# Performance work log

Hardware: AMD Instinct MI355X
Metric: run time of the kernel (lower is better)

The kernel has to match this reference:

```python
import jax, jax.numpy as jnp
import numpy as np

NUM_HEADS = 16
NUM_KV_HEADS = 8
HEAD_DIM = 128
SLIDING_WINDOW = 1024
ROPE_THETA = 10000.0
EPS = 1e-6


def _rms_norm(x, w, eps=EPS):
    # x: [..., head_dim]; Gemma RMSNorm: x * rsqrt(mean(x^2)+eps) * (1 + w)
    var = jnp.mean(jnp.square(x), axis=-1, keepdims=True)
    return x * jax.lax.rsqrt(var + eps) * (1.0 + w)


def _rotate_half(x):
    h = x.shape[-1] // 2
    return jnp.concatenate([-x[..., h:], x[..., :h]], axis=-1)


def _rope_cos_sin(seq_len, dim, theta, dtype):
    inv_freq = 1.0 / (theta ** (jnp.arange(0, dim, 2, dtype=jnp.float32) / dim))
    t = jnp.arange(seq_len, dtype=jnp.float32)
    freqs = jnp.outer(t, inv_freq)              # [S, dim/2]
    emb = jnp.concatenate([freqs, freqs], -1)   # [S, dim]
    return jnp.cos(emb).astype(dtype), jnp.sin(emb).astype(dtype)


def setup_inputs() -> dict:
    key = jax.random.key(0)
    ks = jax.random.split(key, 7)
    B, S, H = 2, 2048, 2048
    std = 0.02
    return {
        "hidden_states": jax.random.normal(ks[0], (B, S, H), jnp.float32),
        "wq": jax.random.normal(ks[1], (NUM_HEADS * HEAD_DIM, H), jnp.float32) * std,
        "wk": jax.random.normal(ks[2], (NUM_KV_HEADS * HEAD_DIM, H), jnp.float32) * std,
        "wv": jax.random.normal(ks[3], (NUM_KV_HEADS * HEAD_DIM, H), jnp.float32) * std,
        "wo": jax.random.normal(ks[4], (H, NUM_HEADS * HEAD_DIM), jnp.float32) * std,
        "q_norm_weight": jnp.zeros((HEAD_DIM,), jnp.float32),
        "k_norm_weight": jnp.zeros((HEAD_DIM,), jnp.float32),
    }


def reference(hidden_states, wq, wk, wv, wo, q_norm_weight, k_norm_weight):
    B, S, H = hidden_states.shape
    # QKV projections (Linear, no bias): x @ W^T
    q = (hidden_states @ wq.T).reshape(B, S, NUM_HEADS, HEAD_DIM).transpose(0, 2, 1, 3)
    k = (hidden_states @ wk.T).reshape(B, S, NUM_KV_HEADS, HEAD_DIM).transpose(0, 2, 1, 3)
    v = (hidden_states @ wv.T).reshape(B, S, NUM_KV_HEADS, HEAD_DIM).transpose(0, 2, 1, 3)
    # QK RMSNorm (per head_dim)
    q = _rms_norm(q, q_norm_weight)
    k = _rms_norm(k, k_norm_weight)
    # RoPE (local layer -> theta=10000)
    cos, sin = _rope_cos_sin(S, HEAD_DIM, ROPE_THETA, q.dtype)  # [S, D]
    q = q * cos + _rotate_half(q) * sin
    k = k * cos + _rotate_half(k) * sin
    # GQA: repeat kv heads (repeat_interleave on head dim)
    groups = NUM_HEADS // NUM_KV_HEADS
    k = jnp.repeat(k, groups, axis=1)
    v = jnp.repeat(v, groups, axis=1)
    # scores [B, H, S, S]
    scale = 1.0 / jnp.sqrt(jnp.asarray(HEAD_DIM, jnp.float32))
    scores = jnp.einsum("bhqd,bhkd->bhqk", q, k) * scale
    # sliding-window causal mask: allowed iff i - window + 1 <= j <= i
    i = jnp.arange(S)[:, None]
    j = jnp.arange(S)[None, :]
    allowed = (j <= i) & (j > i - SLIDING_WINDOW)
    scores = jnp.where(allowed, scores, jnp.float32(-jnp.inf))
    probs = jax.nn.softmax(scores.astype(jnp.float32), axis=-1).astype(q.dtype)
    attn = jnp.einsum("bhqk,bhkd->bhqd", probs, v)  # [B, H, S, D]
    attn = attn.transpose(0, 2, 1, 3).reshape(B, S, NUM_HEADS * HEAD_DIM)
    return attn @ wo.T
```

## Files before the change

### kernel.cpp

```cpp
#include <hip/hip_runtime.h>
#include <stdint.h>
#include <math.h>

typedef unsigned short u16;
typedef __attribute__((ext_vector_type(8))) __bf16 v8bf;
typedef v8bf __attribute__((may_alias)) v8bf_a;
typedef __attribute__((ext_vector_type(4))) float v4f;
typedef __attribute__((ext_vector_type(4))) u16 v4u16;
typedef v4u16 __attribute__((may_alias)) v4u16_a;
typedef __attribute__((ext_vector_type(8))) u16 v8u16;
typedef v8u16 __attribute__((may_alias)) v8u16_a;

__device__ __forceinline__ float bf2f(u16 u) {
    union { uint32_t i; float f; } c; c.i = ((uint32_t)u) << 16; return c.f;
}
__device__ __forceinline__ u16 f2bf(float f) {
    union { float f; uint32_t i; } c; c.f = f;
    return (u16)((c.i + 0x7FFFu + ((c.i >> 16) & 1u)) >> 16);
}
__device__ __forceinline__ void gl_lds16(const u16* g, u16* l) {
    __builtin_amdgcn_global_load_lds(
        (const __attribute__((address_space(1))) void*)g,
        (__attribute__((address_space(3))) void*)l, 16, 0, 0);
}

__global__ __launch_bounds__(256) void convert_bf16(
    const float* __restrict__ src, u16* __restrict__ dst, int n)
{
    const int stride = gridDim.x * blockDim.x;
    for (int i = blockIdx.x * blockDim.x + threadIdx.x; i * 8 < n; i += stride) {
        const int base = i * 8;
        v8u16 o;
#pragma unroll
        for (int j = 0; j < 8; j++) o[j] = f2bf(src[base + j]);
        *(v8u16_a*)(dst + base) = o;
    }
}

template <bool F32OUT>
__global__ __launch_bounds__(256) void gemm_bt(
    const u16* __restrict__ A, int lda,
    const u16* __restrict__ W0, const u16* __restrict__ W1, const u16* __restrict__ W2,
    int n1, int n2, void* __restrict__ Cv, int ldc, int K)
{
    __shared__ __align__(16) u16 As[128 * 32];
    __shared__ __align__(16) u16 Bs[128 * 32];
    const int t  = threadIdx.x;
    const int m0 = blockIdx.x * 128, n0 = blockIdx.y * 128;

    const u16* W; int nw;
    if (n0 < n1)      { W = W0; nw = n0; }
    else if (n0 < n2) { W = W1; nw = n0 - n1; }
    else              { W = W2; nw = n0 - n2; }

    const int lrow = t >> 2, lcol = (t & 3) * 8;
    const u16* gA = A + (size_t)(m0 + lrow) * lda + lcol;
    const u16* gB = W + (size_t)(nw + lrow) * K + lcol;

    const int wid = t >> 6, lane = t & 63;
    const int wm = (wid >> 1) * 64, wn = (wid & 1) * 64;
    const int l15 = lane & 15, quad = lane >> 4;

    v4f acc[4][4] = {};

    for (int k0 = 0; k0 < K; k0 += 32) {
        gl_lds16(gA + k0,                      As + t * 8);
        gl_lds16(gA + k0 + (size_t)64 * lda,   As + 2048 + t * 8);
        gl_lds16(gB + k0,                      Bs + t * 8);
        gl_lds16(gB + k0 + (size_t)64 * K,     Bs + 2048 + t * 8);
        __syncthreads();
        v8bf af[4], bfr[4];
#pragma unroll
        for (int i = 0; i < 4; i++) af[i]  = *(const v8bf_a*)(As + (wm + i * 16 + l15) * 32 + quad * 8);
#pragma unroll
        for (int j = 0; j < 4; j++) bfr[j] = *(const v8bf_a*)(Bs + (wn + j * 16 + l15) * 32 + quad * 8);
#pragma unroll
        for (int i = 0; i < 4; i++)
#pragma unroll
            for (int j = 0; j < 4; j++)
                acc[i][j] = __builtin_amdgcn_mfma_f32_16x16x32_bf16(af[i], bfr[j], acc[i][j], 0, 0, 0);
        __syncthreads();
    }

#pragma unroll
    for (int i = 0; i < 4; i++)
#pragma unroll
        for (int j = 0; j < 4; j++)
#pragma unroll
            for (int r = 0; r < 4; r++) {
                const int row = m0 + wm + i * 16 + quad * 4 + r;
                const int col = n0 + wn + j * 16 + l15;
                if (F32OUT) ((float*)Cv)[(size_t)row * ldc + col] = acc[i][j][r];
                else        ((u16*)Cv)[(size_t)row * ldc + col]   = f2bf(acc[i][j][r]);
            }
}

__global__ __launch_bounds__(256) void normrope(
    u16* __restrict__ qkv, const u16* __restrict__ qw, const u16* __restrict__ kw)
{
    const int tok = blockIdx.x;
    const int s = tok & 2047;
    const int wid = threadIdx.x >> 6, lane = threadIdx.x & 63;
    const int d  = lane * 2;
    const int dm = d & 63;
    const float kln = 9.210340371976184f / 64.f;
    const float inv0 = expf(-(float)dm * kln);
    const float inv1 = expf(-(float)(dm + 1) * kln);
    float sn0, cs0, sn1, cs1;
    __sincosf((float)s * inv0, &sn0, &cs0);
    __sincosf((float)s * inv1, &sn1, &cs1);

    for (int task = wid; task < 24; task += 4) {
        const bool isq = task < 16;
        const int  hh  = isq ? task : task - 16;
        u16* p = qkv + (size_t)tok * 4096 + (isq ? hh * 128 : 2048 + hh * 128) + d;
        const float x0 = bf2f(p[0]), x1 = bf2f(p[1]);
        float ss = x0 * x0 + x1 * x1;
#pragma unroll
        for (int off = 32; off; off >>= 1) ss += __shfl_xor(ss, off);
        const float rr = rsqrtf(ss * (1.f / 128.f) + 1e-6f);
        const u16* wp = (isq ? qw : kw) + d;
        const float xn0 = x0 * rr * (1.f + bf2f(wp[0]));
        const float xn1 = x1 * rr * (1.f + bf2f(wp[1]));
        const float pp0 = __shfl_xor(xn0, 32);
        const float pp1 = __shfl_xor(xn1, 32);
        float o0, o1;
        if (lane < 32) { o0 = xn0 * cs0 - pp0 * sn0; o1 = xn1 * cs1 - pp1 * sn1; }
        else           { o0 = xn0 * cs0 + pp0 * sn0; o1 = xn1 * cs1 + pp1 * sn1; }
        p[0] = f2bf(o0); p[1] = f2bf(o1);
    }
}

__global__ __launch_bounds__(256) void vtrans(
    const u16* __restrict__ qkv, u16* __restrict__ v_t)
{
    __shared__ __align__(16) u16 tile[64][80];
    const int b = blockIdx.x, st = blockIdx.y * 64, ct = blockIdx.z * 64;
    const int t = threadIdx.x;
    {
        const int sl = t >> 2, cq = (t & 3) * 16;
        const u16* src = qkv + ((size_t)(b * 2048 + st + sl)) * 4096 + 3072 + ct + cq;
        *(v8u16_a*)&tile[sl][cq]     = *(const v8u16_a*)src;
        *(v8u16_a*)&tile[sl][cq + 8] = *(const v8u16_a*)(src + 8);
    }
    __syncthreads();
    {
        const int dl = t >> 2, sq = (t & 3) * 16;
        v8u16 o0, o1;
#pragma unroll
        for (int i = 0; i < 8; i++) { o0[i] = tile[sq + i][dl]; o1[i] = tile[sq + 8 + i][dl]; }
        u16* dst = v_t + ((size_t)(b * 1024 + ct + dl)) * 2048 + st + sq;
        *(v8u16_a*)dst       = o0;
        *(v8u16_a*)(dst + 8) = o1;
    }
}

__global__ __launch_bounds__(256) void attn_fa(
    const u16* __restrict__ qkv,
    const u16* __restrict__ v_t,
    u16* __restrict__ attn)
{
    __shared__ __align__(16) u16 Ks[2][32 * 128];
    __shared__ __align__(16) u16 p_lds[4][16 * 72];
    const int bh = blockIdx.x;
    const int b = bh >> 4, h = bh & 15, kvh = h >> 1;
    const int t = threadIdx.x;
    const int wid = t >> 6, lane = t & 63;
    const int l15 = lane & 15, quad = lane >> 4;
    const int qb0 = ((int)gridDim.y - 1 - (int)blockIdx.y) * 64;
    const int qw0 = qb0 + wid * 16;
    const int q   = qw0 + l15;

    const u16* Qb = qkv + ((size_t)(b * 2048 + q)) * 4096 + h * 128 + quad * 8;
    v8bf qf[4];
#pragma unroll
    for (int kc = 0; kc < 4; kc++) qf[kc] = *(const v8bf_a*)(Qb + kc * 32);

    const u16* Kb = qkv + (size_t)b * 2048 * 4096 + 2048 + kvh * 128;
    const u16* Vb = v_t + (size_t)(b * 1024 + kvh * 128) * 2048;

    int ks = qb0 - 1023; if (ks < 0) ks = 0;
    const int kstart = ks & ~31, kend = qb0 + 63;

    const int sr0 = t >> 4, sc = t & 15, sr1 = sr0 + 16;
    const int so0 = (sc ^ (sr0 & 7)) * 8;
    const int so1 = (sc ^ (sr1 & 7)) * 8;

    gl_lds16(Kb + (size_t)(kstart + sr0) * 4096 + so0, &Ks[0][(size_t)t * 8]);
    gl_lds16(Kb + (size_t)(kstart + sr1) * 4096 + so1, &Ks[0][(size_t)(256 + t) * 8]);

    v4f o[8] = {};
    float m_run = -INFINITY;
    float msafe = 0.f;
    float l_i = 0.f;
    const float kSc = 0.08838834764831845f;
    const float THR = 90.50966799187808f;
    u16* P = &p_lds[wid][0];
    const int swz = l15 & 7;

    int buf = 0;
    for (int kt = kstart; kt <= kend; kt += 32, buf ^= 1) {
        __syncthreads();
        if (kt + 32 <= kend) {
            gl_lds16(Kb + (size_t)(kt + 32 + sr0) * 4096 + so0, &Ks[buf ^ 1][(size_t)t * 8]);
            gl_lds16(Kb + (size_t)(kt + 32 + sr1) * 4096 + so1, &Ks[buf ^ 1][(size_t)(256 + t) * 8]);
        }
        if (kt > qw0 + 15 || kt + 31 <= qw0 - 1024) continue;

        v8bf vf[8];
        const u16* Vr = Vb + (size_t)l15 * 2048 + kt + quad * 8;
#pragma unroll
        for (int nt = 0; nt < 8; nt++) vf[nt] = *(const v8bf_a*)(Vr + (size_t)nt * 16 * 2048);

        v4f s0 = {}, s1 = {};
        const u16* K0 = &Ks[buf][(size_t)l15 * 128];
        const u16* K1 = K0 + 16 * 128;
#pragma unroll
        for (int kc = 0; kc < 4; kc++) {
            const int cs = ((kc * 4 + quad) ^ swz) * 8;
            s0 = __builtin_amdgcn_mfma_f32_16x16x32_bf16(*(const v8bf_a*)(K0 + cs), qf[kc], s0, 0, 0, 0);
            s1 = __builtin_amdgcn_mfma_f32_16x16x32_bf16(*(const v8bf_a*)(K1 + cs), qf[kc], s1, 0, 0, 0);
        }

        float p[8];
        float mx = -INFINITY;
#pragma unroll
        for (int r = 0; r < 4; r++) {
            const int kk0 = kt + quad * 4 + r, kk1 = kk0 + 16;
            const float v0 = (kk0 <= q && kk0 > q - 1024) ? s0[r] : -INFINITY;
            const float v1 = (kk1 <= q && kk1 > q - 1024) ? s1[r] : -INFINITY;
            p[r] = v0; p[r + 4] = v1;
            mx = fmaxf(mx, fmaxf(v0, v1));
        }
        mx = fmaxf(mx, __shfl_xor(mx, 16));
        mx = fmaxf(mx, __shfl_xor(mx, 32));

        if (!__all(mx <= m_run + THR)) {
            const float mnew  = fmaxf(m_run, mx);
            const float msn   = (mnew == -INFINITY) ? 0.f : mnew;
            const float alpha = __expf((m_run - msn) * kSc);
#pragma unroll
            for (int nt = 0; nt < 8; nt++)
#pragma unroll
                for (int r = 0; r < 4; r++) o[nt][r] *= alpha;
            l_i *= alpha;
            m_run = mnew; msafe = msn;
        }

        const float mb = msafe * kSc;
        float ps = 0.f;
#pragma unroll
        for (int j = 0; j < 8; j++) {
            p[j] = __expf(__builtin_fmaf(p[j], kSc, -mb));
            ps += p[j];
        }

        union { v4u16 v; uint32_t d[2]; } u0, u1;
        asm("v_cvt_pk_bf16_f32 %0, %1, %2" : "=v"(u0.d[0]) : "v"(p[0]), "v"(p[1]));
        asm("v_cvt_pk_bf16_f32 %0, %1, %2" : "=v"(u0.d[1]) : "v"(p[2]), "v"(p[3]));
        asm("v_cvt_pk_bf16_f32 %0, %1, %2" : "=v"(u1.d[0]) : "v"(p[4]), "v"(p[5]));
        asm("v_cvt_pk_bf16_f32 %0, %1, %2" : "=v"(u1.d[1]) : "v"(p[6]), "v"(p[7]));
        *(v4u16_a*)(P + l15 * 72 + quad * 4)      = u0.v;
        *(v4u16_a*)(P + l15 * 72 + 16 + quad * 4) = u1.v;

        ps += __shfl_xor(ps, 16);
        ps += __shfl_xor(ps, 32);
        l_i += ps;

        asm volatile("s_waitcnt lgkmcnt(0)" ::: "memory");
        const v8bf pf = *(const v8bf_a*)(P + l15 * 72 + quad * 8);
#pragma unroll
        for (int nt = 0; nt < 8; nt++)
            o[nt] = __builtin_amdgcn_mfma_f32_16x16x32_bf16(vf[nt], pf, o[nt], 0, 0, 0);
    }

    const float inv = 1.0f / l_i;
    u16* orow = attn + ((size_t)(b * 2048 + q)) * 2048 + h * 128 + quad * 4;
#pragma unroll
    for (int nt = 0; nt < 8; nt++) {
        v4u16 ov;
#pragma unroll
        for (int r = 0; r < 4; r++) ov[r] = f2bf(o[nt][r] * inv);
        *(v4u16_a*)(orow + nt * 16) = ov;
    }
}

extern "C" void kernel_launch(void* const* d_in, const int* in_sizes, int n_in,
                              void* d_out, int out_size, void* d_ws, size_t ws_size,
                              hipStream_t stream)
{
    u16* qkv  = (u16*)d_ws;
    u16* v_t  = qkv  + (size_t)16777216;
    u16* xa   = v_t  + (size_t)4194304;
    u16* wbf  = xa   + (size_t)8388608;
    u16* nwq  = wbf  + (size_t)8388608;
    u16* nwk  = nwq  + 128;

    convert_bf16<<<4096, 256, 0, stream>>>((const float*)d_in[0], xa,            8388608);
    convert_bf16<<<2048, 256, 0, stream>>>((const float*)d_in[1], wbf,           4194304);
    convert_bf16<<<1024, 256, 0, stream>>>((const float*)d_in[2], wbf + 4194304, 2097152);
    convert_bf16<<<1024, 256, 0, stream>>>((const float*)d_in[3], wbf + 6291456, 2097152);
    convert_bf16<<<1,    256, 0, stream>>>((const float*)d_in[5], nwq,           128);
    convert_bf16<<<1,    256, 0, stream>>>((const float*)d_in[6], nwk,           128);
    gemm_bt<false><<<dim3(32, 32), 256, 0, stream>>>(xa, 2048, wbf, wbf + 4194304, wbf + 6291456,
                                                     2048, 3072, qkv, 4096, 2048);
    convert_bf16<<<2048, 256, 0, stream>>>((const float*)d_in[4], wbf, 4194304);
    normrope<<<dim3(4096), 256, 0, stream>>>(qkv, nwq, nwk);
    vtrans<<<dim3(2, 32, 16), 256, 0, stream>>>(qkv, v_t);
    attn_fa<<<dim3(32, 32), 256, 0, stream>>>(qkv, v_t, xa);
    gemm_bt<true><<<dim3(32, 16), 256, 0, stream>>>(xa, 2048, wbf, wbf, wbf,
                                                    2048, 4096, d_out, 2048, 2048);
}
```

Baseline: 413.2 us.

## Replace GEMM with 256x256-tile, 512-thread, triple-buffered pipelined kernel

```diff
diff --git a/kernel.cpp b/kernel.cpp
--- a/kernel.cpp
+++ b/kernel.cpp
@@ -38,58 +38,82 @@
 }
 
 template <bool F32OUT>
-__global__ __launch_bounds__(256) void gemm_bt(
+__global__ __launch_bounds__(512) void gemm_p3(
     const u16* __restrict__ A, int lda,
     const u16* __restrict__ W0, const u16* __restrict__ W1, const u16* __restrict__ W2,
     int n1, int n2, void* __restrict__ Cv, int ldc, int K)
 {
-    __shared__ __align__(16) u16 As[128 * 32];
-    __shared__ __align__(16) u16 Bs[128 * 32];
+    __shared__ __align__(16) u16 lds[3][16384];
     const int t  = threadIdx.x;
-    const int m0 = blockIdx.x * 128, n0 = blockIdx.y * 128;
+    const int m0 = blockIdx.x * 256, n0 = blockIdx.y * 256;
 
     const u16* W; int nw;
     if (n0 < n1)      { W = W0; nw = n0; }
     else if (n0 < n2) { W = W1; nw = n0 - n1; }
     else              { W = W2; nw = n0 - n2; }
 
-    const int lrow = t >> 2, lcol = (t & 3) * 8;
-    const u16* gA = A + (size_t)(m0 + lrow) * lda + lcol;
-    const u16* gB = W + (size_t)(nw + lrow) * K + lcol;
+    const int c0 = t, c1 = 512 + t;
+    const int ra0 = ((c0 >> 6) << 4) + (c0 & 15), ca0 = ((c0 >> 4) & 3) << 3;
+    const int ra1 = ((c1 >> 6) << 4) + (c1 & 15), ca1 = ((c1 >> 4) & 3) << 3;
+    const u16* sa0 = A + (size_t)(m0 + ra0) * lda + ca0;
+    const u16* sa1 = A + (size_t)(m0 + ra1) * lda + ca1;
+    const u16* sb0 = W + (size_t)(nw + ra0) * K   + ca0;
+    const u16* sb1 = W + (size_t)(nw + ra1) * K   + ca1;
+
+#define STAGE_P3(koff, dst)                                  \
+    do {                                                     \
+        gl_lds16(sa0 + (koff), (dst) + c0 * 8);              \
+        gl_lds16(sa1 + (koff), (dst) + c1 * 8);              \
+        gl_lds16(sb0 + (koff), (dst) + 8192 + c0 * 8);       \
+        gl_lds16(sb1 + (koff), (dst) + 8192 + c1 * 8);       \
+    } while (0)
+
+    const int NT = K >> 5;
+    STAGE_P3(0,  lds[0]);
+    STAGE_P3(32, lds[1]);
 
     const int wid = t >> 6, lane = t & 63;
-    const int wm = (wid >> 1) * 64, wn = (wid & 1) * 64;
     const int l15 = lane & 15, quad = lane >> 4;
-
-    v4f acc[4][4] = {};
-
-    for (int k0 = 0; k0 < K; k0 += 32) {
-        gl_lds16(gA + k0,                      As + t * 8);
-        gl_lds16(gA + k0 + (size_t)64 * lda,   As + 2048 + t * 8);
-        gl_lds16(gB + k0,                      Bs + t * 8);
-        gl_lds16(gB + k0 + (size_t)64 * K,     Bs + 2048 + t * 8);
-        __syncthreads();
-        v8bf af[4], bfr[4];
-#pragma unroll
-        for (int i = 0; i < 4; i++) af[i]  = *(const v8bf_a*)(As + (wm + i * 16 + l15) * 32 + quad * 8);
-#pragma unroll
-        for (int j = 0; j < 4; j++) bfr[j] = *(const v8bf_a*)(Bs + (wn + j * 16 + l15) * 32 + quad * 8);
-#pragma unroll
-        for (int i = 0; i < 4; i++)
+    const int wr8 = (wid >> 2) << 3;
+    const int wc4 = (wid & 3) << 2;
+    const int lofs = lane << 3;
+
+    v4f acc[8][4] = {};
+    int bb = 0;
+    for (int kt = 0; kt < NT; ++kt) {
+        if (kt < NT - 1) asm volatile("s_waitcnt vmcnt(4)" ::: "memory");
+        else             asm volatile("s_waitcnt vmcnt(0)" ::: "memory");
+        __builtin_amdgcn_s_barrier();
+        if (kt + 2 < NT) {
+            int nb = bb + 2; if (nb >= 3) nb -= 3;
+            STAGE_P3((kt + 2) * 32, lds[nb]);
+        }
+        const u16* Ab = lds[bb];
+        const u16* Bb = Ab + 8192;
+        v8bf af[8], bv[4];
+#pragma unroll
+        for (int i = 0; i < 8; i++) af[i] = *(const v8bf_a*)(Ab + ((wr8 + i) << 9) + lofs);
+#pragma unroll
+        for (int j = 0; j < 4; j++) bv[j] = *(const v8bf_a*)(Bb + ((wc4 + j) << 9) + lofs);
+        __builtin_amdgcn_s_setprio(1);
+#pragma unroll
+        for (int i = 0; i < 8; i++)
 #pragma unroll
             for (int j = 0; j < 4; j++)
-                acc[i][j] = __builtin_amdgcn_mfma_f32_16x16x32_bf16(af[i], bfr[j], acc[i][j], 0, 0, 0);
-        __syncthreads();
-    }
-
-#pragma unroll
-    for (int i = 0; i < 4; i++)
+                acc[i][j] = __builtin_amdgcn_mfma_f32_16x16x32_bf16(af[i], bv[j], acc[i][j], 0, 0, 0);
+        __builtin_amdgcn_s_setprio(0);
+        bb = (bb == 2) ? 0 : bb + 1;
+    }
+#undef STAGE_P3
+
+#pragma unroll
+    for (int i = 0; i < 8; i++)
 #pragma unroll
         for (int j = 0; j < 4; j++)
 #pragma unroll
             for (int r = 0; r < 4; r++) {
-                const int row = m0 + wm + i * 16 + quad * 4 + r;
-                const int col = n0 + wn + j * 16 + l15;
+                const int row = m0 + (wr8 + i) * 16 + quad * 4 + r;
+                const int col = n0 + (wc4 + j) * 16 + l15;
                 if (F32OUT) ((float*)Cv)[(size_t)row * ldc + col] = acc[i][j][r];
                 else        ((u16*)Cv)[(size_t)row * ldc + col]   = f2bf(acc[i][j][r]);
             }
@@ -302,12 +326,12 @@
     convert_bf16<<<1024, 256, 0, stream>>>((const float*)d_in[3], wbf + 6291456, 2097152);
     convert_bf16<<<1,    256, 0, stream>>>((const float*)d_in[5], nwq,           128);
     convert_bf16<<<1,    256, 0, stream>>>((const float*)d_in[6], nwk,           128);
-    gemm_bt<false><<<dim3(32, 32), 256, 0, stream>>>(xa, 2048, wbf, wbf + 4194304, wbf + 6291456,
+    gemm_p3<false><<<dim3(16, 16), 512, 0, stream>>>(xa, 2048, wbf, wbf + 4194304, wbf + 6291456,
                                                      2048, 3072, qkv, 4096, 2048);
     convert_bf16<<<2048, 256, 0, stream>>>((const float*)d_in[4], wbf, 4194304);
     normrope<<<dim3(4096), 256, 0, stream>>>(qkv, nwq, nwk);
     vtrans<<<dim3(2, 32, 16), 256, 0, stream>>>(qkv, v_t);
     attn_fa<<<dim3(32, 32), 256, 0, stream>>>(qkv, v_t, xa);
-    gemm_bt<true><<<dim3(32, 16), 256, 0, stream>>>(xa, 2048, wbf, wbf, wbf,
-                                                    2048, 4096, d_out, 2048, 2048);
-}
+    gemm_p3<true><<<dim3(16, 8), 512, 0, stream>>>(xa, 2048, wbf, wbf, wbf,
+                                                   4096, 4096, d_out, 2048, 2048);
+}
```

After: 396.2 us. 4.1% less time.
